# Kernel optimization log

Hardware: AMD Instinct MI355X
Metric: run time of the kernel (lower is better)

## Reference

```python
import jax, jax.numpy as jnp
import numpy as np

B, S, D_IN, D_OUT, H = 8, 512, 1024, 1024, 8
D_ATT = D_OUT // H
NEG_INF = -1e30


def setup_inputs() -> dict:
    key = jax.random.key(0)
    k1, k2, k3, k4 = jax.random.split(key, 4)
    stdv = 1.0 / np.sqrt(D_OUT)
    return {
        "x": jax.random.normal(k1, (B, S, D_IN), dtype=jnp.float32),
        "mask": jnp.ones((B, S), dtype=jnp.float32),
        "adjacency": jax.random.randint(k2, (B, S, S), 0, 2, dtype=jnp.int32),
        "W": jax.random.uniform(k3, (D_IN, D_OUT), dtype=jnp.float32, minval=-stdv, maxval=stdv),
        "att_w": jax.random.normal(k4, (2 * D_ATT,), dtype=jnp.float32) * 0.05,
        "att_b": jnp.zeros((), dtype=jnp.float32),
    }


def reference(x, mask, adjacency, W, att_w, att_b):
    # projection: [B,S,D_IN] @ [D_IN,D_OUT]
    xp = jnp.einsum("bsi,io->bso", x, W)
    # split heads -> [B,H,S,d]
    xh = xp.reshape(B, S, H, D_ATT).transpose(0, 2, 1, 3)
    # LinearMatrixAttention, combination='x,y': sim[i,j] = w1.x_i + w2.x_j + b
    s1 = jnp.einsum("bhsd,d->bhs", xh, att_w[:D_ATT])
    s2 = jnp.einsum("bhsd,d->bhs", xh, att_w[D_ATT:])
    sim = s1[..., :, None] + s2[..., None, :] + att_b  # [B,H,S,S]
    # mask = adjacency AND outer(mask, mask), broadcast over heads
    pair_mask = (adjacency[:, None, :, :] > 0) & (mask[:, None, :, None] > 0) & (mask[:, None, None, :] > 0)
    att = jax.nn.softmax(jnp.where(pair_mask, sim, NEG_INF), axis=-1)
    # weighted sum of values
    out = jnp.einsum("bhij,bhjd->bhid", att, xh)
    out = out.transpose(0, 2, 1, 3).reshape(B, S, D_OUT)
    return out  # activation is identity (None)
```

## Files before the change

### kernel.cpp

```cpp
#include <hip/hip_runtime.h>
#include <hip/hip_bf16.h>

#define B_    8
#define S_    512
#define DIN   1024
#define DOUT  1024
#define H_    8
#define DA    128

using bf16x8 = __attribute__((ext_vector_type(8))) short;
using f32x4  = __attribute__((ext_vector_type(4))) float;

__device__ __forceinline__ ushort f2bf(float f) {
  __hip_bfloat16 h = __float2bfloat16(f);
  return *reinterpret_cast<ushort*>(&h);
}
__device__ __forceinline__ float bf2f(ushort u) {
  union { float f; unsigned int i; } v;
  v.i = ((unsigned int)u) << 16;
  return v.f;
}

__device__ __forceinline__ void gld16(const ushort* g, ushort* l) {
  __builtin_amdgcn_global_load_lds(
      (const __attribute__((address_space(1))) unsigned int*)g,
      (__attribute__((address_space(3))) unsigned int*)l, 16, 0, 0);
}

__global__ __launch_bounds__(256) void k_conv(const float* __restrict__ x,
                                              ushort* __restrict__ xbf, int n) {
  int i = (blockIdx.x * 256 + threadIdx.x) * 8;
  if (i >= n) return;
  const float4* p = reinterpret_cast<const float4*>(x + i);
  float4 a = p[0], b = p[1];
  ushort r[8];
  r[0] = f2bf(a.x); r[1] = f2bf(a.y); r[2] = f2bf(a.z); r[3] = f2bf(a.w);
  r[4] = f2bf(b.x); r[5] = f2bf(b.y); r[6] = f2bf(b.z); r[7] = f2bf(b.w);
  *reinterpret_cast<uint4*>(xbf + i) = *reinterpret_cast<uint4*>(r);
}

__global__ __launch_bounds__(256) void k_wt(const float* __restrict__ W,
                                            ushort* __restrict__ WT) {
  __shared__ float tile[64][65];
  int r0 = blockIdx.y * 64, c0 = blockIdx.x * 64;
  int t = threadIdx.x;
  int lr = t >> 4, lc = (t & 15) * 4;
#pragma unroll
  for (int i = 0; i < 4; ++i) {
    int row = lr + i * 16;
    float4 v = *reinterpret_cast<const float4*>(&W[(size_t)(r0 + row) * DOUT + c0 + lc]);
    tile[row][lc] = v.x; tile[row][lc + 1] = v.y;
    tile[row][lc + 2] = v.z; tile[row][lc + 3] = v.w;
  }
  __syncthreads();
  int n = t >> 2, ks = (t & 3) * 16;
  ushort o[16];
#pragma unroll
  for (int i = 0; i < 16; ++i) o[i] = f2bf(tile[ks + i][n]);
  ushort* dst = &WT[(size_t)(c0 + n) * DIN + r0 + ks];
  reinterpret_cast<uint4*>(dst)[0] = reinterpret_cast<uint4*>(o)[0];
  reinterpret_cast<uint4*>(dst)[1] = reinterpret_cast<uint4*>(o)[1];
}

__global__ __launch_bounds__(256) void k_proj(const ushort* __restrict__ xbf,
                                              const ushort* __restrict__ WT,
                                              ushort* __restrict__ xhT) {
  __shared__ ushort As[128 * 32];
  __shared__ ushort Bs[128 * 32];
  __shared__ ushort Tr[128 * 130];
  int m0 = blockIdx.x * 128;
  int h  = blockIdx.y;
  int t = threadIdx.x;
  int lane = t & 63, wave = t >> 6;
  int wm = wave >> 1, wn = wave & 1;
  int r = t >> 2, c = (t & 3) << 3;

  f32x4 acc[4][4] = {};
  const ushort* ga = &xbf[(size_t)(m0 + r) * DIN + c];
  const ushort* gb = &WT[(size_t)(h * 128 + r) * DIN + c];
  ushort* la = &As[t * 8];
  ushort* lb = &Bs[t * 8];
  int rowa = wm * 64 + (lane & 15);
  int rowb = wn * 64 + (lane & 15);
  int koff = (lane >> 4) * 8;

  for (int kt = 0; kt < DIN; kt += 32) {
    gld16(ga + kt, la);
    gld16(ga + kt + 64 * DIN, la + 2048);
    gld16(gb + kt, lb);
    gld16(gb + kt + 64 * DIN, lb + 2048);
    asm volatile("s_waitcnt vmcnt(0)" ::: "memory");
    __syncthreads();
    bf16x8 a[4], b[4];
#pragma unroll
    for (int mi = 0; mi < 4; ++mi)
      a[mi] = *reinterpret_cast<const bf16x8*>(&As[(rowa + mi * 16) * 32 + koff]);
#pragma unroll
    for (int ni = 0; ni < 4; ++ni)
      b[ni] = *reinterpret_cast<const bf16x8*>(&Bs[(rowb + ni * 16) * 32 + koff]);
#pragma unroll
    for (int mi = 0; mi < 4; ++mi)
#pragma unroll
      for (int ni = 0; ni < 4; ++ni)
        acc[mi][ni] = __builtin_amdgcn_mfma_f32_16x16x32_bf16(a[mi], b[ni], acc[mi][ni], 0, 0, 0);
    __syncthreads();
  }

  int colb = wn * 64 + (lane & 15);
  int rowc = wm * 64 + ((lane >> 4) << 2);
#pragma unroll
  for (int mi = 0; mi < 4; ++mi)
#pragma unroll
    for (int ni = 0; ni < 4; ++ni) {
      int cc = colb + ni * 16;
      int rr = rowc + mi * 16;
#pragma unroll
      for (int j = 0; j < 4; ++j)
        Tr[(rr + j) * 130 + cc] = f2bf(acc[mi][ni][j]);
    }
  __syncthreads();
  int b = m0 >> 9, s0 = m0 & 511;
  int d = t >> 1, sseg = (t & 1) * 64;
  ushort* dst = &xhT[((size_t)(b * H_ + h) * 128 + d) * S_ + s0 + sseg];
#pragma unroll
  for (int g = 0; g < 8; ++g) {
    ushort o[8];
#pragma unroll
    for (int i = 0; i < 8; ++i) o[i] = Tr[(sseg + g * 8 + i) * 130 + d];
    reinterpret_cast<uint4*>(dst)[g] = *reinterpret_cast<uint4*>(o);
  }
}

__global__ __launch_bounds__(512) void k_s2(const ushort* __restrict__ xhT,
                                            const float* __restrict__ attw,
                                            const float* __restrict__ mask,
                                            ushort* __restrict__ ubf) {
  int bh = blockIdx.x;
  int j = threadIdx.x;
  int b = bh >> 3;
  const ushort* base = &xhT[(size_t)bh * 128 * S_ + j];
  float s = 0.f;
#pragma unroll 8
  for (int d = 0; d < 128; ++d)
    s += bf2f(base[(size_t)d * S_]) * attw[128 + d];
  __shared__ float red[512];
  red[j] = s;
  __syncthreads();
  for (int off = 256; off > 0; off >>= 1) {
    if (j < off) red[j] = fmaxf(red[j], red[j + off]);
    __syncthreads();
  }
  float mx = red[0];
  float u = (mask[b * S_ + j] > 0.f) ? __expf(s - mx) : 0.f;
  ubf[bh * S_ + j] = f2bf(u);
}

__global__ __launch_bounds__(256) void k_attn(const int* __restrict__ adj,
                                              const ushort* __restrict__ xhT,
                                              const ushort* __restrict__ ubf,
                                              float* __restrict__ out) {
  __shared__ ushort As[128 * 32];
  __shared__ ushort Bs[128 * 32];
  __shared__ ushort us[512];
  __shared__ float Dred[256];
  int i0 = blockIdx.x * 128;
  int h  = blockIdx.y;
  int b  = blockIdx.z;
  int t = threadIdx.x, lane = t & 63, wave = t >> 6;
  int wm = wave >> 1, wn = wave & 1;

  if (t < 256)
    reinterpret_cast<unsigned int*>(us)[t] =
        reinterpret_cast<const unsigned int*>(&ubf[(b * H_ + h) * S_])[t];
  __syncthreads();

  int ir = t >> 1;
  int c0 = (t & 1) * 16;
  const int* arow = &adj[((size_t)(b * S_ + i0 + ir)) * S_ + c0];
  const ushort* gv = &xhT[((size_t)(b * H_ + h) * 128 + (t >> 2)) * S_ + ((t & 3) << 3)];
  ushort* lb = &Bs[t * 8];
  float dacc = 0.f;
  f32x4 acc[4][4] = {};
  int rowa = wm * 64 + (lane & 15);
  int rowb = wn * 64 + (lane & 15);
  int koff = (lane >> 4) * 8;

  for (int kt = 0; kt < S_; kt += 32) {
    __syncthreads();
    gld16(gv + kt, lb);
    gld16(gv + kt + 64 * S_, lb + 2048);
    int ai[16];
    *reinterpret_cast<int4*>(ai)      = *reinterpret_cast<const int4*>(arow + kt);
    *reinterpret_cast<int4*>(ai + 4)  = *reinterpret_cast<const int4*>(arow + kt + 4);
    *reinterpret_cast<int4*>(ai + 8)  = *reinterpret_cast<const int4*>(arow + kt + 8);
    *reinterpret_cast<int4*>(ai + 12) = *reinterpret_cast<const int4*>(arow + kt + 12);
    ushort av[16];
#pragma unroll
    for (int q = 0; q < 16; ++q) {
      ushort uq = us[kt + c0 + q];
      bool nz = (ai[q] != 0);
      av[q] = nz ? uq : (ushort)0;
      dacc += nz ? bf2f(uq) : 0.f;
    }
    *reinterpret_cast<uint4*>(&As[ir * 32 + c0])     = reinterpret_cast<uint4*>(av)[0];
    *reinterpret_cast<uint4*>(&As[ir * 32 + c0 + 8]) = reinterpret_cast<uint4*>(av)[1];
    asm volatile("s_waitcnt vmcnt(0)" ::: "memory");
    __syncthreads();
    bf16x8 a[4], bfr[4];
#pragma unroll
    for (int mi = 0; mi < 4; ++mi)
      a[mi] = *reinterpret_cast<const bf16x8*>(&As[(rowa + mi * 16) * 32 + koff]);
#pragma unroll
    for (int ni = 0; ni < 4; ++ni)
      bfr[ni] = *reinterpret_cast<const bf16x8*>(&Bs[(rowb + ni * 16) * 32 + koff]);
#pragma unroll
    for (int mi = 0; mi < 4; ++mi)
#pragma unroll
      for (int ni = 0; ni < 4; ++ni)
        acc[mi][ni] = __builtin_amdgcn_mfma_f32_16x16x32_bf16(a[mi], bfr[ni], acc[mi][ni], 0, 0, 0);
  }

  Dred[t] = dacc;
  __syncthreads();

  int rowc = wm * 64 + ((lane >> 4) << 2);
  int colb = wn * 64 + (lane & 15);
#pragma unroll
  for (int mi = 0; mi < 4; ++mi)
#pragma unroll
    for (int ni = 0; ni < 4; ++ni) {
      int cc = colb + ni * 16;
#pragma unroll
      for (int j = 0; j < 4; ++j) {
        int rr = rowc + mi * 16 + j;
        float Di = Dred[rr * 2] + Dred[rr * 2 + 1];
        Di = fmaxf(Di, 1e-30f);
        out[((size_t)(b * S_ + i0 + rr)) * DOUT + h * 128 + cc] = acc[mi][ni][j] / Di;
      }
    }
}

extern "C" void kernel_launch(void* const* d_in, const int* in_sizes, int n_in,
                              void* d_out, int out_size, void* d_ws, size_t ws_size,
                              hipStream_t stream) {
  const float* x    = (const float*)d_in[0];
  const float* mask = (const float*)d_in[1];
  const int*   adj  = (const int*)d_in[2];
  const float* W    = (const float*)d_in[3];
  const float* attw = (const float*)d_in[4];
  float* out = (float*)d_out;

  char* ws = (char*)d_ws;
  ushort* xbf = (ushort*)ws;
  ushort* WT  = (ushort*)(ws + 8388608);
  ushort* xhT = (ushort*)(ws + 10485760);
  ushort* ubf = (ushort*)(ws + 18874368);

  k_conv<<<dim3(2048), dim3(256), 0, stream>>>(x, xbf, B_ * S_ * DIN);
  k_wt<<<dim3(16, 16), dim3(256), 0, stream>>>(W, WT);
  k_proj<<<dim3(32, 8), dim3(256), 0, stream>>>(xbf, WT, xhT);
  k_s2<<<dim3(64), dim3(512), 0, stream>>>(xhT, attw, mask, ubf);
  k_attn<<<dim3(4, 8, 8), dim3(256), 0, stream>>>(adj, xhT, ubf, out);
}
```

Before: 137.2 us.

## Fuse prep kernels, bit-pack adjacency, fold s2 into projection, halve tile sizes

Merges the x conversion, W transpose and a new adjacency-to-bitmask pass into one launch, and folds the s2 score and exp computation into the projection epilogue. It drops the row-max subtraction, relying on the softmax shift invariance, which risks overflow if scores grow large. Projection and attention tiles shrink to 64 rows with K=64 per iteration, doubling the grid for better CU occupancy. The attention kernel reads a 64-bit mask word per row segment instead of 16 int32 adjacency values per thread, cutting adjacency traffic to 1/32.

After: 118.8 us. -13.4%, faster.

```diff
diff --git a/kernel.cpp b/kernel.cpp
--- a/kernel.cpp
+++ b/kernel.cpp
@@ -6,7 +6,6 @@
 #define DIN   1024
 #define DOUT  1024
 #define H_    8
-#define DA    128
 
 using bf16x8 = __attribute__((ext_vector_type(8))) short;
 using f32x4  = __attribute__((ext_vector_type(4))) float;
@@ -27,214 +26,239 @@
       (__attribute__((address_space(3))) unsigned int*)l, 16, 0, 0);
 }
 
-__global__ __launch_bounds__(256) void k_conv(const float* __restrict__ x,
-                                              ushort* __restrict__ xbf, int n) {
-  int i = (blockIdx.x * 256 + threadIdx.x) * 8;
-  if (i >= n) return;
-  const float4* p = reinterpret_cast<const float4*>(x + i);
-  float4 a = p[0], b = p[1];
-  ushort r[8];
-  r[0] = f2bf(a.x); r[1] = f2bf(a.y); r[2] = f2bf(a.z); r[3] = f2bf(a.w);
-  r[4] = f2bf(b.x); r[5] = f2bf(b.y); r[6] = f2bf(b.z); r[7] = f2bf(b.w);
-  *reinterpret_cast<uint4*>(xbf + i) = *reinterpret_cast<uint4*>(r);
-}
-
-__global__ __launch_bounds__(256) void k_wt(const float* __restrict__ W,
-                                            ushort* __restrict__ WT) {
+__global__ __launch_bounds__(256) void k_prep(const float* __restrict__ x,
+                                              ushort* __restrict__ xbf,
+                                              const float* __restrict__ W,
+                                              ushort* __restrict__ WT,
+                                              const int* __restrict__ adj,
+                                              unsigned long long* __restrict__ bm) {
   __shared__ float tile[64][65];
-  int r0 = blockIdx.y * 64, c0 = blockIdx.x * 64;
+  int blk = blockIdx.x;
   int t = threadIdx.x;
-  int lr = t >> 4, lc = (t & 15) * 4;
-#pragma unroll
-  for (int i = 0; i < 4; ++i) {
-    int row = lr + i * 16;
-    float4 v = *reinterpret_cast<const float4*>(&W[(size_t)(r0 + row) * DOUT + c0 + lc]);
-    tile[row][lc] = v.x; tile[row][lc + 1] = v.y;
-    tile[row][lc + 2] = v.z; tile[row][lc + 3] = v.w;
-  }
-  __syncthreads();
-  int n = t >> 2, ks = (t & 3) * 16;
-  ushort o[16];
-#pragma unroll
-  for (int i = 0; i < 16; ++i) o[i] = f2bf(tile[ks + i][n]);
-  ushort* dst = &WT[(size_t)(c0 + n) * DIN + r0 + ks];
-  reinterpret_cast<uint4*>(dst)[0] = reinterpret_cast<uint4*>(o)[0];
-  reinterpret_cast<uint4*>(dst)[1] = reinterpret_cast<uint4*>(o)[1];
+  if (blk < 2048) {
+    int i = (blk * 256 + t) * 8;
+    const float4* p = reinterpret_cast<const float4*>(x + i);
+    float4 a = p[0], b = p[1];
+    ushort r[8];
+    r[0] = f2bf(a.x); r[1] = f2bf(a.y); r[2] = f2bf(a.z); r[3] = f2bf(a.w);
+    r[4] = f2bf(b.x); r[5] = f2bf(b.y); r[6] = f2bf(b.z); r[7] = f2bf(b.w);
+    *reinterpret_cast<uint4*>(xbf + i) = *reinterpret_cast<uint4*>(r);
+  } else if (blk < 2304) {
+    int q = blk - 2048;
+    int r0 = (q >> 4) * 64, c0 = (q & 15) * 64;
+    int lr = t >> 4, lc = (t & 15) * 4;
+#pragma unroll
+    for (int i = 0; i < 4; ++i) {
+      int row = lr + i * 16;
+      float4 v = *reinterpret_cast<const float4*>(&W[(size_t)(r0 + row) * DOUT + c0 + lc]);
+      tile[row][lc] = v.x; tile[row][lc + 1] = v.y;
+      tile[row][lc + 2] = v.z; tile[row][lc + 3] = v.w;
+    }
+    __syncthreads();
+    int n = t >> 2, ks = (t & 3) * 16;
+    ushort o[16];
+#pragma unroll
+    for (int i = 0; i < 16; ++i) o[i] = f2bf(tile[ks + i][n]);
+    ushort* dst = &WT[(size_t)(c0 + n) * DIN + r0 + ks];
+    reinterpret_cast<uint4*>(dst)[0] = reinterpret_cast<uint4*>(o)[0];
+    reinterpret_cast<uint4*>(dst)[1] = reinterpret_cast<uint4*>(o)[1];
+  } else {
+    int w = (blk - 2304) * 4 + (t >> 6);
+    int lane = t & 63;
+    int v = adj[(size_t)w * 64 + lane];
+    unsigned long long m = __ballot(v != 0);
+    if (lane == 0) bm[w] = m;
+  }
 }
 
 __global__ __launch_bounds__(256) void k_proj(const ushort* __restrict__ xbf,
                                               const ushort* __restrict__ WT,
-                                              ushort* __restrict__ xhT) {
-  __shared__ ushort As[128 * 32];
-  __shared__ ushort Bs[128 * 32];
-  __shared__ ushort Tr[128 * 130];
-  int m0 = blockIdx.x * 128;
+                                              const float* __restrict__ attw,
+                                              const float* __restrict__ mask,
+                                              ushort* __restrict__ xhT,
+                                              ushort* __restrict__ ubf) {
+  __shared__ __align__(16) ushort As[2 * 64 * 32];
+  __shared__ __align__(16) ushort Bs[2 * 128 * 32];
+  __shared__ __align__(16) ushort Tr[64 * 130];
+  __shared__ float Pp[64 * 4];
+  int m0 = blockIdx.x * 64;
   int h  = blockIdx.y;
-  int t = threadIdx.x;
-  int lane = t & 63, wave = t >> 6;
-  int wm = wave >> 1, wn = wave & 1;
-  int r = t >> 2, c = (t & 3) << 3;
-
-  f32x4 acc[4][4] = {};
-  const ushort* ga = &xbf[(size_t)(m0 + r) * DIN + c];
-  const ushort* gb = &WT[(size_t)(h * 128 + r) * DIN + c];
-  ushort* la = &As[t * 8];
-  ushort* lb = &Bs[t * 8];
-  int rowa = wm * 64 + (lane & 15);
-  int rowb = wn * 64 + (lane & 15);
-  int koff = (lane >> 4) * 8;
-
-  for (int kt = 0; kt < DIN; kt += 32) {
-    gld16(ga + kt, la);
-    gld16(ga + kt + 64 * DIN, la + 2048);
-    gld16(gb + kt, lb);
-    gld16(gb + kt + 64 * DIN, lb + 2048);
+  int t = threadIdx.x, lane = t & 63, wave = t >> 6;
+  int r4 = t >> 2, c8 = (t & 3) << 3;
+
+  const ushort* ga = &xbf[(size_t)(m0 + r4) * DIN + c8];
+  const ushort* gb = &WT[(size_t)(h * 128 + r4) * DIN + c8];
+  ushort* laA = As + t * 8;
+  ushort* laB = Bs + t * 8;
+  int rowa = lane & 15, koff = (lane >> 4) * 8;
+  int rbb = wave * 32 + (lane & 15);
+
+  f32x4 acc[4][2] = {};
+
+  for (int kt = 0; kt < DIN; kt += 64) {
+    gld16(ga + kt,                laA);
+    gld16(ga + kt + 32,           laA + 2048);
+    gld16(gb + kt,                laB);
+    gld16(gb + kt + 64 * DIN,     laB + 2048);
+    gld16(gb + kt + 32,           laB + 4096);
+    gld16(gb + kt + 32 + 64 * DIN,laB + 6144);
     asm volatile("s_waitcnt vmcnt(0)" ::: "memory");
     __syncthreads();
-    bf16x8 a[4], b[4];
-#pragma unroll
-    for (int mi = 0; mi < 4; ++mi)
-      a[mi] = *reinterpret_cast<const bf16x8*>(&As[(rowa + mi * 16) * 32 + koff]);
-#pragma unroll
-    for (int ni = 0; ni < 4; ++ni)
-      b[ni] = *reinterpret_cast<const bf16x8*>(&Bs[(rowb + ni * 16) * 32 + koff]);
-#pragma unroll
-    for (int mi = 0; mi < 4; ++mi)
-#pragma unroll
-      for (int ni = 0; ni < 4; ++ni)
-        acc[mi][ni] = __builtin_amdgcn_mfma_f32_16x16x32_bf16(a[mi], b[ni], acc[mi][ni], 0, 0, 0);
-    __syncthreads();
-  }
-
-  int colb = wn * 64 + (lane & 15);
-  int rowc = wm * 64 + ((lane >> 4) << 2);
+    bf16x8 a[4][2], bfr[2][2];
+#pragma unroll
+    for (int mi = 0; mi < 4; ++mi)
+#pragma unroll
+      for (int ks = 0; ks < 2; ++ks)
+        a[mi][ks] = *reinterpret_cast<const bf16x8*>(&As[ks * 2048 + (rowa + mi * 16) * 32 + koff]);
+#pragma unroll
+    for (int ni = 0; ni < 2; ++ni)
+#pragma unroll
+      for (int ks = 0; ks < 2; ++ks)
+        bfr[ni][ks] = *reinterpret_cast<const bf16x8*>(&Bs[ks * 4096 + (rbb + ni * 16) * 32 + koff]);
+#pragma unroll
+    for (int mi = 0; mi < 4; ++mi)
+#pragma unroll
+      for (int ni = 0; ni < 2; ++ni)
+#pragma unroll
+        for (int ks = 0; ks < 2; ++ks)
+          acc[mi][ni] = __builtin_amdgcn_mfma_f32_16x16x32_bf16(a[mi][ks], bfr[ni][ks], acc[mi][ni], 0, 0, 0);
+    __syncthreads();
+  }
+
+  int colb = wave * 32 + (lane & 15);
+  int rl = (lane >> 4) * 4;
 #pragma unroll
   for (int mi = 0; mi < 4; ++mi)
 #pragma unroll
-    for (int ni = 0; ni < 4; ++ni) {
+    for (int ni = 0; ni < 2; ++ni) {
       int cc = colb + ni * 16;
-      int rr = rowc + mi * 16;
 #pragma unroll
       for (int j = 0; j < 4; ++j)
-        Tr[(rr + j) * 130 + cc] = f2bf(acc[mi][ni][j]);
-    }
-  __syncthreads();
+        Tr[(mi * 16 + rl + j) * 130 + cc] = f2bf(acc[mi][ni][j]);
+    }
+  __syncthreads();
+
   int b = m0 >> 9, s0 = m0 & 511;
-  int d = t >> 1, sseg = (t & 1) * 64;
-  ushort* dst = &xhT[((size_t)(b * H_ + h) * 128 + d) * S_ + s0 + sseg];
-#pragma unroll
-  for (int g = 0; g < 8; ++g) {
-    ushort o[8];
-#pragma unroll
-    for (int i = 0; i < 8; ++i) o[i] = Tr[(sseg + g * 8 + i) * 130 + d];
-    reinterpret_cast<uint4*>(dst)[g] = *reinterpret_cast<uint4*>(o);
-  }
-}
-
-__global__ __launch_bounds__(512) void k_s2(const ushort* __restrict__ xhT,
-                                            const float* __restrict__ attw,
-                                            const float* __restrict__ mask,
-                                            ushort* __restrict__ ubf) {
-  int bh = blockIdx.x;
-  int j = threadIdx.x;
-  int b = bh >> 3;
-  const ushort* base = &xhT[(size_t)bh * 128 * S_ + j];
-  float s = 0.f;
+  {
+    int row = t >> 2, seg = (t & 3) * 32;
+    float p = 0.f;
 #pragma unroll 8
-  for (int d = 0; d < 128; ++d)
-    s += bf2f(base[(size_t)d * S_]) * attw[128 + d];
-  __shared__ float red[512];
-  red[j] = s;
-  __syncthreads();
-  for (int off = 256; off > 0; off >>= 1) {
-    if (j < off) red[j] = fmaxf(red[j], red[j + off]);
-    __syncthreads();
-  }
-  float mx = red[0];
-  float u = (mask[b * S_ + j] > 0.f) ? __expf(s - mx) : 0.f;
-  ubf[bh * S_ + j] = f2bf(u);
-}
-
-__global__ __launch_bounds__(256) void k_attn(const int* __restrict__ adj,
+    for (int d = 0; d < 32; ++d)
+      p += bf2f(Tr[row * 130 + seg + d]) * attw[128 + seg + d];
+    Pp[row * 4 + (t & 3)] = p;
+  }
+  {
+    int d = t >> 1, sseg = (t & 1) * 32;
+    ushort* dst = &xhT[((size_t)(b * H_ + h) * 128 + d) * S_ + s0 + sseg];
+#pragma unroll
+    for (int g = 0; g < 4; ++g) {
+      ushort o[8];
+#pragma unroll
+      for (int i = 0; i < 8; ++i) o[i] = Tr[(sseg + g * 8 + i) * 130 + d];
+      reinterpret_cast<uint4*>(dst)[g] = *reinterpret_cast<uint4*>(o);
+    }
+  }
+  __syncthreads();
+  if (t < 64) {
+    float s2 = Pp[t * 4] + Pp[t * 4 + 1] + Pp[t * 4 + 2] + Pp[t * 4 + 3];
+    float mk = mask[b * S_ + s0 + t];
+    float u = (mk > 0.f) ? __expf(s2) : 0.f;
+    ubf[(b * H_ + h) * S_ + s0 + t] = f2bf(u);
+  }
+}
+
+__global__ __launch_bounds__(256) void k_attn(const unsigned long long* __restrict__ bm,
                                               const ushort* __restrict__ xhT,
                                               const ushort* __restrict__ ubf,
                                               float* __restrict__ out) {
-  __shared__ ushort As[128 * 32];
-  __shared__ ushort Bs[128 * 32];
-  __shared__ ushort us[512];
-  __shared__ float Dred[256];
-  int i0 = blockIdx.x * 128;
+  __shared__ __align__(16) ushort As[2 * 64 * 32];
+  __shared__ __align__(16) ushort Bs[2 * 128 * 32];
+  __shared__ __align__(16) ushort us[512];
+  __shared__ float Dred[64 * 4];
+  __shared__ float Dsum[64];
+  int i0 = blockIdx.x * 64;
   int h  = blockIdx.y;
   int b  = blockIdx.z;
   int t = threadIdx.x, lane = t & 63, wave = t >> 6;
-  int wm = wave >> 1, wn = wave & 1;
-
-  if (t < 256)
-    reinterpret_cast<unsigned int*>(us)[t] =
-        reinterpret_cast<const unsigned int*>(&ubf[(b * H_ + h) * S_])[t];
-  __syncthreads();
-
-  int ir = t >> 1;
-  int c0 = (t & 1) * 16;
-  const int* arow = &adj[((size_t)(b * S_ + i0 + ir)) * S_ + c0];
-  const ushort* gv = &xhT[((size_t)(b * H_ + h) * 128 + (t >> 2)) * S_ + ((t & 3) << 3)];
-  ushort* lb = &Bs[t * 8];
+
+  if (t < 64)
+    reinterpret_cast<uint4*>(us)[t] =
+        reinterpret_cast<const uint4*>(&ubf[(b * H_ + h) * S_])[t];
+
+  int r4 = t >> 2, c8 = (t & 3) << 3;
+  const ushort* gv = &xhT[((size_t)(b * H_ + h) * 128 + r4) * S_ + c8];
+  ushort* laB = Bs + t * 8;
+
+  int arow = t >> 2, cseg = (t & 3) * 16;
+  const unsigned long long* bmrow = &bm[(size_t)(b * S_ + i0 + arow) * 8];
+  ushort* aw = As + ((cseg >= 32) ? 2048 : 0) + arow * 32 + (cseg & 31);
+
   float dacc = 0.f;
-  f32x4 acc[4][4] = {};
-  int rowa = wm * 64 + (lane & 15);
-  int rowb = wn * 64 + (lane & 15);
-  int koff = (lane >> 4) * 8;
-
-  for (int kt = 0; kt < S_; kt += 32) {
-    __syncthreads();
-    gld16(gv + kt, lb);
-    gld16(gv + kt + 64 * S_, lb + 2048);
-    int ai[16];
-    *reinterpret_cast<int4*>(ai)      = *reinterpret_cast<const int4*>(arow + kt);
-    *reinterpret_cast<int4*>(ai + 4)  = *reinterpret_cast<const int4*>(arow + kt + 4);
-    *reinterpret_cast<int4*>(ai + 8)  = *reinterpret_cast<const int4*>(arow + kt + 8);
-    *reinterpret_cast<int4*>(ai + 12) = *reinterpret_cast<const int4*>(arow + kt + 12);
+  f32x4 acc[4][2] = {};
+  int rowa = lane & 15, koff = (lane >> 4) * 8;
+  int rbb = wave * 32 + (lane & 15);
+
+  __syncthreads();
+
+  for (int kt = 0; kt < S_; kt += 64) {
+    gld16(gv + kt,               laB);
+    gld16(gv + kt + 64 * S_,     laB + 2048);
+    gld16(gv + kt + 32,          laB + 4096);
+    gld16(gv + kt + 32 + 64 * S_,laB + 6144);
+    unsigned long long w = bmrow[kt >> 6];
+    unsigned int bits = (unsigned int)(w >> cseg) & 0xffffu;
+    ushort uu[16];
+    *reinterpret_cast<uint4*>(uu)     = *reinterpret_cast<const uint4*>(&us[kt + cseg]);
+    *reinterpret_cast<uint4*>(uu + 8) = *reinterpret_cast<const uint4*>(&us[kt + cseg + 8]);
     ushort av[16];
 #pragma unroll
     for (int q = 0; q < 16; ++q) {
-      ushort uq = us[kt + c0 + q];
-      bool nz = (ai[q] != 0);
-      av[q] = nz ? uq : (ushort)0;
-      dacc += nz ? bf2f(uq) : 0.f;
-    }
-    *reinterpret_cast<uint4*>(&As[ir * 32 + c0])     = reinterpret_cast<uint4*>(av)[0];
-    *reinterpret_cast<uint4*>(&As[ir * 32 + c0 + 8]) = reinterpret_cast<uint4*>(av)[1];
+      bool nz = (bits >> q) & 1;
+      av[q] = nz ? uu[q] : (ushort)0;
+      dacc += nz ? bf2f(uu[q]) : 0.f;
+    }
+    *reinterpret_cast<uint4*>(aw)     = *reinterpret_cast<uint4*>(av);
+    *reinterpret_cast<uint4*>(aw + 8) = *reinterpret_cast<uint4*>(av + 8);
     asm volatile("s_waitcnt vmcnt(0)" ::: "memory");
     __syncthreads();
-    bf16x8 a[4], bfr[4];
-#pragma unroll
-    for (int mi = 0; mi < 4; ++mi)
-      a[mi] = *reinterpret_cast<const bf16x8*>(&As[(rowa + mi * 16) * 32 + koff]);
-#pragma unroll
-    for (int ni = 0; ni < 4; ++ni)
-      bfr[ni] = *reinterpret_cast<const bf16x8*>(&Bs[(rowb + ni * 16) * 32 + koff]);
-#pragma unroll
-    for (int mi = 0; mi < 4; ++mi)
-#pragma unroll
-      for (int ni = 0; ni < 4; ++ni)
-        acc[mi][ni] = __builtin_amdgcn_mfma_f32_16x16x32_bf16(a[mi], bfr[ni], acc[mi][ni], 0, 0, 0);
-  }
-
-  Dred[t] = dacc;
-  __syncthreads();
-
-  int rowc = wm * 64 + ((lane >> 4) << 2);
-  int colb = wn * 64 + (lane & 15);
+    bf16x8 a[4][2], bfr[2][2];
+#pragma unroll
+    for (int mi = 0; mi < 4; ++mi)
+#pragma unroll
+      for (int ks = 0; ks < 2; ++ks)
+        a[mi][ks] = *reinterpret_cast<const bf16x8*>(&As[ks * 2048 + (rowa + mi * 16) * 32 + koff]);
+#pragma unroll
+    for (int ni = 0; ni < 2; ++ni)
+#pragma unroll
+      for (int ks = 0; ks < 2; ++ks)
+        bfr[ni][ks] = *reinterpret_cast<const bf16x8*>(&Bs[ks * 4096 + (rbb + ni * 16) * 32 + koff]);
+#pragma unroll
+    for (int mi = 0; mi < 4; ++mi)
+#pragma unroll
+      for (int ni = 0; ni < 2; ++ni)
+#pragma unroll
+        for (int ks = 0; ks < 2; ++ks)
+          acc[mi][ni] = __builtin_amdgcn_mfma_f32_16x16x32_bf16(a[mi][ks], bfr[ni][ks], acc[mi][ni], 0, 0, 0);
+    __syncthreads();
+  }
+
+  Dred[arow * 4 + (t & 3)] = dacc;
+  __syncthreads();
+  if (t < 64)
+    Dsum[t] = Dred[t * 4] + Dred[t * 4 + 1] + Dred[t * 4 + 2] + Dred[t * 4 + 3];
+  __syncthreads();
+
+  int colb = wave * 32 + (lane & 15);
+  int rl = (lane >> 4) * 4;
 #pragma unroll
   for (int mi = 0; mi < 4; ++mi)
 #pragma unroll
-    for (int ni = 0; ni < 4; ++ni) {
+    for (int ni = 0; ni < 2; ++ni) {
       int cc = colb + ni * 16;
 #pragma unroll
       for (int j = 0; j < 4; ++j) {
-        int rr = rowc + mi * 16 + j;
-        float Di = Dred[rr * 2] + Dred[rr * 2 + 1];
-        Di = fmaxf(Di, 1e-30f);
+        int rr = mi * 16 + rl + j;
+        float Di = fmaxf(Dsum[rr], 1e-30f);
         out[((size_t)(b * S_ + i0 + rr)) * DOUT + h * 128 + cc] = acc[mi][ni][j] / Di;
       }
     }
@@ -255,10 +279,9 @@
   ushort* WT  = (ushort*)(ws + 8388608);
   ushort* xhT = (ushort*)(ws + 10485760);
   ushort* ubf = (ushort*)(ws + 18874368);
-
-  k_conv<<<dim3(2048), dim3(256), 0, stream>>>(x, xbf, B_ * S_ * DIN);
-  k_wt<<<dim3(16, 16), dim3(256), 0, stream>>>(W, WT);
-  k_proj<<<dim3(32, 8), dim3(256), 0, stream>>>(xbf, WT, xhT);
-  k_s2<<<dim3(64), dim3(512), 0, stream>>>(xhT, attw, mask, ubf);
-  k_attn<<<dim3(4, 8, 8), dim3(256), 0, stream>>>(adj, xhT, ubf, out);
-}
+  unsigned long long* bm = (unsigned long long*)(ws + 18939904);
+
+  k_prep<<<dim3(10496), dim3(256), 0, stream>>>(x, xbf, W, WT, adj, bm);
+  k_proj<<<dim3(64, 8), dim3(256), 0, stream>>>(xbf, WT, attw, mask, xhT, ubf);
+  k_attn<<<dim3(8, 8, 8), dim3(256), 0, stream>>>(bm, xhT, ubf, out);
+}
```
